# Optimization experiments

Hardware: AMD Instinct MI355X
Metric: run time of the kernel (lower is better)

Reference implementation:

```python
import jax, jax.numpy as jnp
import numpy as np

MARGIN = 0.1
SCALE_POS = 2.0
SCALE_NEG = 50.0
THRESH = 0.5
EPS = 1e-5


def setup_inputs() -> dict:
    key = jax.random.key(0)
    k1, k2 = jax.random.split(key)
    feats = jax.random.normal(k1, (4096, 2, 192), dtype=jnp.float32)
    labels = jax.random.randint(k2, (4096,), 0, 4096, dtype=jnp.int64)
    return {"feats": feats, "labels": labels}


def reference(feats, labels):
    B, n_utt, D = feats.shape
    lab = jnp.repeat(labels, n_utt)            # [N]
    f = feats.reshape(-1, D)                   # [N, D]
    N = f.shape[0]

    sim = f @ f.T                              # [N, N]
    # F.normalize(sim): L2-normalize each row, eps=1e-12
    row_norm = jnp.maximum(jnp.linalg.norm(sim, axis=1, keepdims=True), 1e-12)
    S = sim / row_norm

    same = lab[None, :] == lab[:, None]        # [N, N]
    pos_mask = same & (S < 1.0 - EPS)          # pos_pair_ (includes self if < 1-eps)
    neg_mask = ~same                           # neg_pair_

    min_pos = jnp.min(jnp.where(pos_mask, S, jnp.inf), axis=1)    # per-row min(pos_pair_)
    max_neg = jnp.max(jnp.where(neg_mask, S, -jnp.inf), axis=1)   # per-row max(neg_pair_)

    neg_keep = neg_mask & (S > (min_pos - MARGIN)[:, None])
    pos_keep = pos_mask & (S < (max_neg + MARGIN)[:, None])

    has_neg = jnp.any(neg_keep, axis=1)
    has_pos = jnp.any(pos_keep, axis=1)
    valid = has_neg & has_pos

    pos_sum = jnp.sum(jnp.where(pos_keep, jnp.exp(-SCALE_POS * (S - THRESH)), 0.0), axis=1)
    neg_sum = jnp.sum(jnp.where(neg_keep, jnp.exp(SCALE_NEG * (S - THRESH)), 0.0), axis=1)

    row_loss = (1.0 / SCALE_POS) * jnp.log1p(pos_sum) + (1.0 / SCALE_NEG) * jnp.log1p(neg_sum)
    loss = jnp.sum(jnp.where(valid, row_loss, 0.0)) / N

    # prec1 = percent of rows skipped for having no surviving negatives
    prec1 = jnp.sum(~has_neg).astype(jnp.float32) * 100.0 / N
    return loss, prec1
```

## Files before the change

### kernel.cpp

```cpp
#include <hip/hip_runtime.h>
#include <math.h>

typedef float  f32x4  __attribute__((ext_vector_type(4)));
typedef int    int8v  __attribute__((ext_vector_type(8)));

constexpr float MARGIN    = 0.1f;
constexpr float SCALE_POS = 2.0f;
constexpr float SCALE_NEG = 50.0f;
constexpr float THRESH    = 0.5f;
constexpr float ONE_EPS   = 1.0f - 1e-5f;
constexpr float LOG2E     = 1.4426950408889634f;
constexpr float BC        = -(SCALE_NEG * THRESH * LOG2E);
constexpr float VCUT_COEF = (36.0674f - 30.0f) / (SCALE_NEG * LOG2E);

constexpr int D      = 192;
constexpr int KP     = 256;
constexpr int RT     = 4;
constexpr int RPW    = 64;
constexpr int RPB    = 256;
constexpr int CSPLIT = 16;

constexpr int NSLOT  = 32;
constexpr int CBLK   = 256;
constexpr int NTILES = CBLK / 16;
constexpr int NPAIR  = (NSLOT * (NSLOT - 1)) / 2;

constexpr int TILE_B8 = 4096;
constexpr int SCALE1  = 0x7f7f7f7f;

__device__ inline float fast_exp2(float x) {
#if __has_builtin(__builtin_amdgcn_exp2f)
  return __builtin_amdgcn_exp2f(x);
#else
  return exp2f(x);
#endif
}

__device__ inline void pin_frag8(int8v& v) {
  asm volatile("" : "+v"(v));
}

__global__ __launch_bounds__(1024) void k_prep(
    const float* __restrict__ f, unsigned char* __restrict__ pk8, int nrows,
    const int* __restrict__ labs, int* __restrict__ hist_g, int* __restrict__ offs_g,
    int* __restrict__ bucket, float* __restrict__ accum, int n)
{
  if (blockIdx.x < 64) {
    int gid = blockIdx.x * 1024 + threadIdx.x;
    int r = gid >> 3, j = gid & 7;
    if (r >= nrows) return;
    float x[32];
    if (j < 6) {
      const float* src = f + (size_t)r * D + j * 32;
#pragma unroll
      for (int i = 0; i < 8; ++i) {
        float4 v = *(const float4*)(src + i * 4);
        x[i * 4 + 0] = v.x; x[i * 4 + 1] = v.y; x[i * 4 + 2] = v.z; x[i * 4 + 3] = v.w;
      }
    } else {
#pragma unroll
      for (int i = 0; i < 32; ++i) x[i] = 0.f;
    }
    union { int s[8]; int8v v; } u;
#pragma unroll
    for (int i = 0; i < 8; ++i) {
      int p = __builtin_amdgcn_cvt_pk_fp8_f32(x[i * 4 + 0], x[i * 4 + 1], 0, false);
      p     = __builtin_amdgcn_cvt_pk_fp8_f32(x[i * 4 + 2], x[i * 4 + 3], p, true);
      u.s[i] = p;
    }
    int tile = r >> 4, c = r & 15, g = j >> 2, qq = j & 3;
    *(int8v*)(pk8 + (size_t)tile * TILE_B8 + g * 2048 + (qq * 16 + c) * 32) = u.v;
    return;
  }

  __shared__ int histL[4096];
  __shared__ int offsL[4096];
  __shared__ int scanb[1024];
  const int t = threadIdx.x;

  if (t < 3) accum[t] = 0.f;
  for (int i = t; i < 4096; i += 1024) histL[i] = 0;
  __syncthreads();
  for (int i = t; i < n; i += 1024) atomicAdd(&histL[labs[i]], 1);
  __syncthreads();
  int base = t * 4;
  int v[4]; int ls = 0;
  for (int k = 0; k < 4; ++k) { v[k] = ls; ls += histL[base + k]; }
  scanb[t] = ls;
  __syncthreads();
  for (int o = 1; o < 1024; o <<= 1) {
    int x = (t >= o) ? scanb[t - o] : 0;
    __syncthreads();
    scanb[t] += x;
    __syncthreads();
  }
  int ebase = scanb[t] - ls;
  for (int k = 0; k < 4; ++k) {
    offsL[base + k] = ebase + v[k];
    offs_g[base + k] = ebase + v[k];
    hist_g[base + k] = histL[base + k];
  }
  __syncthreads();
  for (int i = t; i < 4096; i += 1024) histL[i] = 0;
  __syncthreads();
  for (int i = t; i < n; i += 1024) {
    int lab = labs[i];
    int p = atomicAdd(&histL[lab], 1);
    bucket[offsL[lab] + p] = i;
  }
}

__global__ __launch_bounds__(256, 2) void k_pass1(
    const unsigned char* __restrict__ pk8, const int* __restrict__ labs,
    float* __restrict__ sumsqP, float* __restrict__ maxnegP, int N)
{
  __shared__ int   ldsLab[CBLK];
  __shared__ float colS[4][CBLK];
  __shared__ float colM[4][CBLK];

  const int tid  = threadIdx.x;
  const int lane = tid & 63;
  const int w    = tid >> 6;
  const int q    = lane >> 4;
  const int c    = lane & 15;

  int i, j;
  if ((int)blockIdx.x < NPAIR) {
    int t = blockIdx.x; i = 0;
    while (t >= NSLOT - 1 - i) { t -= NSLOT - 1 - i; ++i; }
    j = i + 1 + t;
  } else {
    i = j = blockIdx.x - NPAIR;
  }
  const bool offd = (i != j);
  const int rowbase = i * CBLK + w * RPW;
  const int ctile0  = j * NTILES;

  ldsLab[tid] = labs[(j * CBLK + tid) >> 1];

  int8v afr[RT][2];
#pragma unroll
  for (int rt = 0; rt < RT; ++rt)
#pragma unroll
    for (int g = 0; g < 2; ++g) {
      afr[rt][g] = *(const int8v*)(pk8 + (size_t)((rowbase >> 4) + rt) * TILE_B8 + g * 2048 + lane * 32);
      pin_frag8(afr[rt][g]);
    }

  int labrow[RT][4];
#pragma unroll
  for (int rt = 0; rt < RT; ++rt)
#pragma unroll
    for (int rr = 0; rr < 4; ++rr)
      labrow[rt][rr] = labs[(rowbase + rt * 16 + q * 4 + rr) >> 1];

  float ssq[RT][4], mxn[RT][4];
#pragma unroll
  for (int rt = 0; rt < RT; ++rt)
#pragma unroll
    for (int rr = 0; rr < 4; ++rr) { ssq[rt][rr] = 0.f; mxn[rt][rr] = -INFINITY; }

  __syncthreads();

  auto loadB = [&](int tile, int8v (&bf)[2]) {
    const unsigned char* bp = pk8 + (size_t)(ctile0 + tile) * TILE_B8 + lane * 32;
#pragma unroll
    for (int g = 0; g < 2; ++g) bf[g] = *(const int8v*)(bp + g * 2048);
  };
  auto compute = [&](const int8v (&bf)[2], int t) {
    const int labcol = ldsLab[t * 16 + c];
    f32x4 acc[RT];
#pragma unroll
    for (int rt = 0; rt < RT; ++rt) acc[rt] = 0.f;
#pragma unroll
    for (int g = 0; g < 2; ++g)
#pragma unroll
      for (int rt = 0; rt < RT; ++rt)
        acc[rt] = __builtin_amdgcn_mfma_scale_f32_16x16x128_f8f6f4(
            afr[rt][g], bf[g], acc[rt], 0, 0, 0, SCALE1, 0, SCALE1);
    float csA = 0.f, cmA = -INFINITY;
#pragma unroll
    for (int rt = 0; rt < RT; ++rt)
#pragma unroll
      for (int rr = 0; rr < 4; ++rr) {
        float v = acc[rt][rr];
        ssq[rt][rr] = fmaf(v, v, ssq[rt][rr]);
        float vm = (labrow[rt][rr] == labcol) ? -INFINITY : v;
        mxn[rt][rr] = fmaxf(mxn[rt][rr], vm);
        csA = fmaf(v, v, csA);
        cmA = fmaxf(cmA, vm);
      }
    if (offd) {
      csA += __shfl_xor(csA, 16, 64);
      csA += __shfl_xor(csA, 32, 64);
      cmA = fmaxf(cmA, __shfl_xor(cmA, 16, 64));
      cmA = fmaxf(cmA, __shfl_xor(cmA, 32, 64));
      if (q == 0) { colS[w][t * 16 + c] = csA; colM[w][t * 16 + c] = cmA; }
    }
  };

  int8v b0[2], b1[2];
  loadB(0, b0);
  for (int t = 0; t < NTILES; t += 2) {
    loadB(t + 1, b1);
    compute(b0, t);
    int nx = t + 2; nx = (nx < NTILES) ? nx : 0;
    loadB(nx, b0);
    compute(b1, t + 1);
  }

#pragma unroll
  for (int rt = 0; rt < RT; ++rt)
#pragma unroll
    for (int rr = 0; rr < 4; ++rr) {
      float s = ssq[rt][rr], m = mxn[rt][rr];
#pragma unroll
      for (int msk = 1; msk < 16; msk <<= 1) {
        s += __shfl_xor(s, msk, 64);
        m = fmaxf(m, __shfl_xor(m, msk, 64));
      }
      if (c == 0) {
        int row = rowbase + rt * 16 + q * 4 + rr;
        sumsqP[(size_t)j * N + row] = s;
        maxnegP[(size_t)j * N + row] = m;
      }
    }

  if (offd) {
    __syncthreads();
    float s4 = colS[0][tid] + colS[1][tid] + colS[2][tid] + colS[3][tid];
    float m4 = fmaxf(fmaxf(colM[0][tid], colM[1][tid]),
                     fmaxf(colM[2][tid], colM[3][tid]));
    const int colrow = j * CBLK + tid;
    sumsqP[(size_t)i * N + colrow] = s4;
    maxnegP[(size_t)i * N + colrow] = m4;
  }
}

__global__ void k_rowstats(
    const float* __restrict__ f, const int* __restrict__ labs,
    const float* __restrict__ sumsqP, const float* __restrict__ maxnegP,
    const int* __restrict__ offs, const int* __restrict__ hist, const int* __restrict__ bucket,
    float* __restrict__ nthr2, float* __restrict__ arow,
    float* __restrict__ validf, float* __restrict__ hasnegf, float* __restrict__ posloss,
    int N)
{
  const int lane = threadIdx.x & 63;
  const int row  = blockIdx.x * 4 + (threadIdx.x >> 6);

  float s = 0.f, m = -INFINITY;
  if (lane < NSLOT) {
    s = sumsqP[(size_t)lane * N + row];
    m = maxnegP[(size_t)lane * N + row];
  }
#pragma unroll
  for (int msk = 1; msk < 64; msk <<= 1) {
    s += __shfl_xor(s, msk, 64);
    m = fmaxf(m, __shfl_xor(m, msk, 64));
  }
  float nrm = fmaxf(sqrtf(s), 1e-12f);
  float inv = 1.0f / nrm;
  float maxnegS = m * inv;
  float posth = fminf(ONE_EPS, maxnegS + MARGIN);

  const int lab = labs[row >> 1];
  const int beg = offs[lab], cnt = hist[lab];
  const float* fi = f + (size_t)row * D;
  float x0 = fi[lane], x1 = fi[lane + 64], x2 = fi[lane + 128];

  float minp = INFINITY, psum = 0.f; int pcnt = 0;
  for (int t = 0; t < cnt; ++t) {
    int smp = bucket[beg + t];
#pragma unroll
    for (int u = 0; u < 2; ++u) {
      const float* fj = f + (size_t)(smp * 2 + u) * D;
      float p = x0 * fj[lane] + x1 * fj[lane + 64] + x2 * fj[lane + 128];
#pragma unroll
      for (int msk = 1; msk < 64; msk <<= 1) p += __shfl_xor(p, msk, 64);
      minp = fminf(minp, p);
      float S = p * inv;
      if (S < posth) {
        psum += fast_exp2((THRESH - S) * (SCALE_POS * LOG2E));
        pcnt++;
      }
    }
  }

  float minS = minp * inv;
  float min_pos = (minS < ONE_EPS) ? minS : INFINITY;
  bool hneg = maxnegS > (min_pos - MARGIN);
  bool valid = hneg && (pcnt > 0);
  if (lane == 0) {
    nthr2[row]   = fmaxf((min_pos - MARGIN) * nrm, VCUT_COEF * nrm);
    arow[row]    = inv * (SCALE_NEG * LOG2E);
    validf[row]  = valid ? 1.f : 0.f;
    hasnegf[row] = hneg ? 1.f : 0.f;
    posloss[row] = valid ? ((1.0f / SCALE_POS) * log1pf(psum)) : 0.f;
  }
}

__global__ __launch_bounds__(256, 2) void k_pass2(
    const unsigned char* __restrict__ pk8,
    const float* __restrict__ nthr2, const float* __restrict__ arow,
    const float* __restrict__ maxnegP,
    float* __restrict__ negsumP, int N, int cps)
{
  const int lane = threadIdx.x & 63;
  const int w    = threadIdx.x >> 6;
  const int q    = lane >> 4;
  const int c    = lane & 15;
  const int cs   = blockIdx.x & (CSPLIT - 1);
  const int rbb  = blockIdx.x / CSPLIT;
  const int rowbase = rbb * RPB + w * RPW;
  const int ctile0 = (cs * cps) >> 4;
  const int ntiles = cps >> 4;

  {
    int myrow = rowbase + lane;
    float mn = fmaxf(maxnegP[(size_t)(2 * cs) * N + myrow],
                     maxnegP[(size_t)(2 * cs + 1) * N + myrow]);
    float th = nthr2[myrow];
    unsigned long long bal = __ballot(mn > th);
    if (bal == 0ull) {
      negsumP[(size_t)cs * N + myrow] = 0.f;
      return;
    }
  }

  int8v afr[RT][2];
#pragma unroll
  for (int rt = 0; rt < RT; ++rt)
#pragma unroll
    for (int g = 0; g < 2; ++g) {
      afr[rt][g] = *(const int8v*)(pk8 + (size_t)((rowbase >> 4) + rt) * TILE_B8 + g * 2048 + lane * 32);
      pin_frag8(afr[rt][g]);
    }

  float nthrv[RT][4], arw[RT][4], ns[RT][4];
#pragma unroll
  for (int rt = 0; rt < RT; ++rt)
#pragma unroll
    for (int rr = 0; rr < 4; ++rr) {
      int row = rowbase + rt * 16 + q * 4 + rr;
      nthrv[rt][rr] = nthr2[row];
      arw[rt][rr]   = arow[row];
      ns[rt][rr]    = 0.f;
    }

  auto loadB = [&](int tile, int8v (&bf)[2]) {
    const unsigned char* bp = pk8 + (size_t)(ctile0 + tile) * TILE_B8 + lane * 32;
#pragma unroll
    for (int g = 0; g < 2; ++g) bf[g] = *(const int8v*)(bp + g * 2048);
  };
  auto compute = [&](const int8v (&bf)[2]) {
    f32x4 acc[RT];
#pragma unroll
    for (int rt = 0; rt < RT; ++rt) acc[rt] = 0.f;
#pragma unroll
    for (int g = 0; g < 2; ++g)
#pragma unroll
      for (int rt = 0; rt < RT; ++rt)
        acc[rt] = __builtin_amdgcn_mfma_scale_f32_16x16x128_f8f6f4(
            afr[rt][g], bf[g], acc[rt], 0, 0, 0, SCALE1, 0, SCALE1);
#pragma unroll
    for (int rt = 0; rt < RT; ++rt)
#pragma unroll
      for (int rr = 0; rr < 4; ++rr) {
        float v = acc[rt][rr];
        float e = fast_exp2(fmaf(v, arw[rt][rr], BC));
        ns[rt][rr] += (v > nthrv[rt][rr]) ? e : 0.f;
      }
  };

  int8v b0[2], b1[2];
  loadB(0, b0);
  for (int t = 0; t < ntiles; t += 2) {
    loadB(t + 1, b1);
    compute(b0);
    int nx = t + 2; nx = (nx < ntiles) ? nx : 0;
    loadB(nx, b0);
    compute(b1);
  }

#pragma unroll
  for (int rt = 0; rt < RT; ++rt)
#pragma unroll
    for (int rr = 0; rr < 4; ++rr) {
      float sv = ns[rt][rr];
#pragma unroll
      for (int msk = 1; msk < 16; msk <<= 1) sv += __shfl_xor(sv, msk, 64);
      if (c == 0) {
        int row = rowbase + rt * 16 + q * 4 + rr;
        negsumP[(size_t)cs * N + row] = sv;
      }
    }
}

__global__ void k_final(const float* __restrict__ negsumP, const float* __restrict__ posloss,
                        const float* __restrict__ validf, const float* __restrict__ hasnegf,
                        float* __restrict__ accum, float* __restrict__ out, int N)
{
  int i = blockIdx.x * blockDim.x + threadIdx.x;
  float lacc = 0.f, nacc = 0.f;
  if (i < N) {
    float nsum = 0.f;
    for (int cs2 = 0; cs2 < CSPLIT; ++cs2) nsum += negsumP[(size_t)cs2 * N + i];
    lacc = validf[i] * (posloss[i] + (1.0f / SCALE_NEG) * log1pf(nsum));
    nacc = 1.0f - hasnegf[i];
  }
#pragma unroll
  for (int msk = 1; msk < 64; msk <<= 1) {
    lacc += __shfl_xor(lacc, msk, 64);
    nacc += __shfl_xor(nacc, msk, 64);
  }
  __shared__ float sl[4], sn[4];
  __shared__ bool isLast;
  int wid = threadIdx.x >> 6, lane = threadIdx.x & 63;
  if (lane == 0) { sl[wid] = lacc; sn[wid] = nacc; }
  __syncthreads();
  if (threadIdx.x == 0) {
    float L = sl[0] + sl[1] + sl[2] + sl[3];
    float Nn = sn[0] + sn[1] + sn[2] + sn[3];
    atomicAdd(&accum[0], L);
    atomicAdd(&accum[1], Nn);
    __threadfence();
    int tkt = atomicAdd((int*)&accum[2], 1);
    isLast = (tkt == (int)gridDim.x - 1);
  }
  __syncthreads();
  if (isLast && threadIdx.x == 0) {
    __threadfence();
    out[0] = accum[0] / (float)N;
    out[1] = accum[1] * 100.0f / (float)N;
  }
}

extern "C" void kernel_launch(void* const* d_in, const int* in_sizes, int n_in,
                              void* d_out, int out_size, void* d_ws, size_t ws_size,
                              hipStream_t stream)
{
  (void)n_in; (void)out_size; (void)ws_size;
  const float* f    = (const float*)d_in[0];
  const int*   labs = (const int*)d_in[1];
  const int Bs = in_sizes[1];
  const int N  = 2 * Bs;

  char* ws = (char*)d_ws;
  size_t off = 0;
  auto alloc = [&](size_t bytes) -> void* {
    void* p = ws + off;
    off += (bytes + 255) & ~(size_t)255;
    return p;
  };
  unsigned char* pk8 = (unsigned char*)alloc((size_t)N * KP);
  float* sumsqP  = (float*)alloc((size_t)NSLOT * N * sizeof(float));
  float* maxnegP = (float*)alloc((size_t)NSLOT * N * sizeof(float));
  float* negsumP = sumsqP;
  float* nthr2   = (float*)alloc((size_t)N * sizeof(float));
  float* arow    = (float*)alloc((size_t)N * sizeof(float));
  float* validf  = (float*)alloc((size_t)N * sizeof(float));
  float* hasnegf = (float*)alloc((size_t)N * sizeof(float));
  float* posloss = (float*)alloc((size_t)N * sizeof(float));
  int* hist   = (int*)alloc((size_t)Bs * sizeof(int));
  int* offs   = (int*)alloc((size_t)Bs * sizeof(int));
  int* bucket = (int*)alloc((size_t)Bs * sizeof(int));
  float* accum = (float*)alloc(4 * sizeof(float));

  k_prep<<<65, 1024, 0, stream>>>(f, pk8, N, labs, hist, offs, bucket, accum, Bs);

  k_pass1<<<NPAIR + NSLOT, 256, 0, stream>>>(pk8, labs, sumsqP, maxnegP, N);
  k_rowstats<<<N / 4, 256, 0, stream>>>(f, labs, sumsqP, maxnegP, offs, hist, bucket,
                                        nthr2, arow, validf, hasnegf, posloss, N);
  const int cps   = N / CSPLIT;
  const int grid2 = (N / RPB) * CSPLIT;
  k_pass2<<<grid2, 256, 0, stream>>>(pk8, nthr2, arow, maxnegP, negsumP, N, cps);
  k_final<<<N / 256, 256, 0, stream>>>(negsumP, posloss, validf, hasnegf, accum, (float*)d_out, N);
}
```

Baseline: 106.0 us.

## Split pass1 tile pairs into column halves and double pass2 column split

Each symmetric block-pair in pass1 is now split across two workgroups, each handling half of the 256 column tiles. Row and column partial sums go to separate buffers, indexed so rowstats and pass2 can pick the right source. Pass2's column split doubles to 32 so each block handles one 256-column slab, which lines up the early-skip check with pass1's per-slab maxneg partials. This is meant to raise parallelism and occupancy on the many-CU GPU. In exchange, partial-buffer traffic and the number of reduction slots grow.

Result: slower. 112.1 us (+5.7%).

```diff
diff --git a/kernel.cpp b/kernel.cpp
--- a/kernel.cpp
+++ b/kernel.cpp
@@ -18,11 +18,12 @@
 constexpr int RT     = 4;
 constexpr int RPW    = 64;
 constexpr int RPB    = 256;
-constexpr int CSPLIT = 16;
+constexpr int CSPLIT = 32;
 
 constexpr int NSLOT  = 32;
 constexpr int CBLK   = 256;
 constexpr int NTILES = CBLK / 16;
+constexpr int HT     = 8;
 constexpr int NPAIR  = (NSLOT * (NSLOT - 1)) / 2;
 
 constexpr int TILE_B8 = 4096;
@@ -112,11 +113,12 @@
 
 __global__ __launch_bounds__(256, 2) void k_pass1(
     const unsigned char* __restrict__ pk8, const int* __restrict__ labs,
-    float* __restrict__ sumsqP, float* __restrict__ maxnegP, int N)
-{
-  __shared__ int   ldsLab[CBLK];
-  __shared__ float colS[4][CBLK];
-  __shared__ float colM[4][CBLK];
+    float* __restrict__ rowPs, float* __restrict__ rowPm,
+    float* __restrict__ colPs, float* __restrict__ colPm, int N)
+{
+  __shared__ int   ldsLab[128];
+  __shared__ float colS[4][128];
+  __shared__ float colM[4][128];
 
   const int tid  = threadIdx.x;
   const int lane = tid & 63;
@@ -124,19 +126,21 @@
   const int q    = lane >> 4;
   const int c    = lane & 15;
 
+  const int pid = blockIdx.x >> 1;
+  const int h   = blockIdx.x & 1;
   int i, j;
-  if ((int)blockIdx.x < NPAIR) {
-    int t = blockIdx.x; i = 0;
+  if (pid < NPAIR) {
+    int t = pid; i = 0;
     while (t >= NSLOT - 1 - i) { t -= NSLOT - 1 - i; ++i; }
     j = i + 1 + t;
   } else {
-    i = j = blockIdx.x - NPAIR;
+    i = j = pid - NPAIR;
   }
   const bool offd = (i != j);
   const int rowbase = i * CBLK + w * RPW;
-  const int ctile0  = j * NTILES;
-
-  ldsLab[tid] = labs[(j * CBLK + tid) >> 1];
+  const int ctile0  = j * NTILES + h * HT;
+
+  if (tid < 128) ldsLab[tid] = labs[(j * CBLK + h * 128 + tid) >> 1];
 
   int8v afr[RT][2];
 #pragma unroll
@@ -201,14 +205,15 @@
 
   int8v b0[2], b1[2];
   loadB(0, b0);
-  for (int t = 0; t < NTILES; t += 2) {
+  for (int t = 0; t < HT; t += 2) {
     loadB(t + 1, b1);
     compute(b0, t);
-    int nx = t + 2; nx = (nx < NTILES) ? nx : 0;
+    int nx = t + 2; nx = (nx < HT) ? nx : 0;
     loadB(nx, b0);
     compute(b1, t + 1);
   }
 
+  const int fslot = 2 * j + h;
 #pragma unroll
   for (int rt = 0; rt < RT; ++rt)
 #pragma unroll
@@ -221,25 +226,28 @@
       }
       if (c == 0) {
         int row = rowbase + rt * 16 + q * 4 + rr;
-        sumsqP[(size_t)j * N + row] = s;
-        maxnegP[(size_t)j * N + row] = m;
+        rowPs[(size_t)fslot * N + row] = s;
+        rowPm[(size_t)fslot * N + row] = m;
       }
     }
 
   if (offd) {
     __syncthreads();
-    float s4 = colS[0][tid] + colS[1][tid] + colS[2][tid] + colS[3][tid];
-    float m4 = fmaxf(fmaxf(colM[0][tid], colM[1][tid]),
-                     fmaxf(colM[2][tid], colM[3][tid]));
-    const int colrow = j * CBLK + tid;
-    sumsqP[(size_t)i * N + colrow] = s4;
-    maxnegP[(size_t)i * N + colrow] = m4;
+    if (tid < 128) {
+      float s4 = colS[0][tid] + colS[1][tid] + colS[2][tid] + colS[3][tid];
+      float m4 = fmaxf(fmaxf(colM[0][tid], colM[1][tid]),
+                       fmaxf(colM[2][tid], colM[3][tid]));
+      const int colrow = j * CBLK + h * 128 + tid;
+      colPs[(size_t)i * N + colrow] = s4;
+      colPm[(size_t)i * N + colrow] = m4;
+    }
   }
 }
 
 __global__ void k_rowstats(
     const float* __restrict__ f, const int* __restrict__ labs,
-    const float* __restrict__ sumsqP, const float* __restrict__ maxnegP,
+    const float* __restrict__ rowPs, const float* __restrict__ rowPm,
+    const float* __restrict__ colPs, const float* __restrict__ colPm,
     const int* __restrict__ offs, const int* __restrict__ hist, const int* __restrict__ bucket,
     float* __restrict__ nthr2, float* __restrict__ arow,
     float* __restrict__ validf, float* __restrict__ hasnegf, float* __restrict__ posloss,
@@ -247,11 +255,16 @@
 {
   const int lane = threadIdx.x & 63;
   const int row  = blockIdx.x * 4 + (threadIdx.x >> 6);
+  const int b    = row >> 8;
 
   float s = 0.f, m = -INFINITY;
-  if (lane < NSLOT) {
-    s = sumsqP[(size_t)lane * N + row];
-    m = maxnegP[(size_t)lane * N + row];
+  if (lane >= 2 * b) {
+    s += rowPs[(size_t)lane * N + row];
+    m = fmaxf(m, rowPm[(size_t)lane * N + row]);
+  }
+  if (lane < b) {
+    s += colPs[(size_t)lane * N + row];
+    m = fmaxf(m, colPm[(size_t)lane * N + row]);
   }
 #pragma unroll
   for (int msk = 1; msk < 64; msk <<= 1) {
@@ -302,8 +315,8 @@
 __global__ __launch_bounds__(256, 2) void k_pass2(
     const unsigned char* __restrict__ pk8,
     const float* __restrict__ nthr2, const float* __restrict__ arow,
-    const float* __restrict__ maxnegP,
-    float* __restrict__ negsumP, int N, int cps)
+    const float* __restrict__ rowPm, const float* __restrict__ colPm,
+    float* __restrict__ negsumP, int N)
 {
   const int lane = threadIdx.x & 63;
   const int w    = threadIdx.x >> 6;
@@ -312,13 +325,16 @@
   const int cs   = blockIdx.x & (CSPLIT - 1);
   const int rbb  = blockIdx.x / CSPLIT;
   const int rowbase = rbb * RPB + w * RPW;
-  const int ctile0 = (cs * cps) >> 4;
-  const int ntiles = cps >> 4;
+  const int ctile0 = cs * NTILES;
+  const int ntiles = NTILES;
 
   {
     int myrow = rowbase + lane;
-    float mn = fmaxf(maxnegP[(size_t)(2 * cs) * N + myrow],
-                     maxnegP[(size_t)(2 * cs + 1) * N + myrow]);
+    int b = myrow >> 8;
+    float mn = (cs >= b)
+        ? fmaxf(rowPm[(size_t)(2 * cs) * N + myrow],
+                rowPm[(size_t)(2 * cs + 1) * N + myrow])
+        : colPm[(size_t)cs * N + myrow];
     float th = nthr2[myrow];
     unsigned long long bal = __ballot(mn > th);
     if (bal == 0ull) {
@@ -453,9 +469,11 @@
     return p;
   };
   unsigned char* pk8 = (unsigned char*)alloc((size_t)N * KP);
-  float* sumsqP  = (float*)alloc((size_t)NSLOT * N * sizeof(float));
-  float* maxnegP = (float*)alloc((size_t)NSLOT * N * sizeof(float));
-  float* negsumP = sumsqP;
+  float* rowPs  = (float*)alloc((size_t)64 * N * sizeof(float));
+  float* rowPm  = (float*)alloc((size_t)64 * N * sizeof(float));
+  float* colPs  = (float*)alloc((size_t)NSLOT * N * sizeof(float));
+  float* colPm  = (float*)alloc((size_t)NSLOT * N * sizeof(float));
+  float* negsumP = (float*)alloc((size_t)CSPLIT * N * sizeof(float));
   float* nthr2   = (float*)alloc((size_t)N * sizeof(float));
   float* arow    = (float*)alloc((size_t)N * sizeof(float));
   float* validf  = (float*)alloc((size_t)N * sizeof(float));
@@ -468,11 +486,11 @@
 
   k_prep<<<65, 1024, 0, stream>>>(f, pk8, N, labs, hist, offs, bucket, accum, Bs);
 
-  k_pass1<<<NPAIR + NSLOT, 256, 0, stream>>>(pk8, labs, sumsqP, maxnegP, N);
-  k_rowstats<<<N / 4, 256, 0, stream>>>(f, labs, sumsqP, maxnegP, offs, hist, bucket,
+  k_pass1<<<2 * NPAIR + 2 * NSLOT, 256, 0, stream>>>(pk8, labs, rowPs, rowPm, colPs, colPm, N);
+  k_rowstats<<<N / 4, 256, 0, stream>>>(f, labs, rowPs, rowPm, colPs, colPm,
+                                        offs, hist, bucket,
                                         nthr2, arow, validf, hasnegf, posloss, N);
-  const int cps   = N / CSPLIT;
   const int grid2 = (N / RPB) * CSPLIT;
-  k_pass2<<<grid2, 256, 0, stream>>>(pk8, nthr2, arow, maxnegP, negsumP, N, cps);
+  k_pass2<<<grid2, 256, 0, stream>>>(pk8, nthr2, arow, rowPm, colPm, negsumP, N);
   k_final<<<N / 256, 256, 0, stream>>>(negsumP, posloss, validf, hasnegf, accum, (float*)d_out, N);
 }
```

## Triple-buffer B tiles in pass1 and defer column reduction to LDS

Applied to the files above, without the earlier changes.

In the fused similarity pass, the double-buffered B-tile loop becomes a fully unrolled triple-buffered loop that prefetches two tiles ahead, so global loads can overlap more MFMA work. The per-tile cross-lane shuffle reduction for column statistics is replaced by storing each quad's partials to a larger LDS array and reducing them once at the end. The min-occupancy hint in launch_bounds is dropped so the compiler can use more registers. In exchange it uses more registers and LDS, which may reduce waves per CU.

Measured after the change: 151.5 us. +42.8%, slower.

```diff
diff --git a/kernel.cpp b/kernel.cpp
--- a/kernel.cpp
+++ b/kernel.cpp
@@ -110,13 +110,13 @@
   }
 }
 
-__global__ __launch_bounds__(256, 2) void k_pass1(
+__global__ __launch_bounds__(256) void k_pass1(
     const unsigned char* __restrict__ pk8, const int* __restrict__ labs,
     float* __restrict__ sumsqP, float* __restrict__ maxnegP, int N)
 {
   __shared__ int   ldsLab[CBLK];
-  __shared__ float colS[4][CBLK];
-  __shared__ float colM[4][CBLK];
+  __shared__ float colS[4][4][CBLK];
+  __shared__ float colM[4][4][CBLK];
 
   const int tid  = threadIdx.x;
   const int lane = tid & 63;
@@ -191,22 +191,19 @@
         cmA = fmaxf(cmA, vm);
       }
     if (offd) {
-      csA += __shfl_xor(csA, 16, 64);
-      csA += __shfl_xor(csA, 32, 64);
-      cmA = fmaxf(cmA, __shfl_xor(cmA, 16, 64));
-      cmA = fmaxf(cmA, __shfl_xor(cmA, 32, 64));
-      if (q == 0) { colS[w][t * 16 + c] = csA; colM[w][t * 16 + c] = cmA; }
+      colS[w][q][t * 16 + c] = csA;
+      colM[w][q][t * 16 + c] = cmA;
     }
   };
 
-  int8v b0[2], b1[2];
-  loadB(0, b0);
-  for (int t = 0; t < NTILES; t += 2) {
-    loadB(t + 1, b1);
-    compute(b0, t);
-    int nx = t + 2; nx = (nx < NTILES) ? nx : 0;
-    loadB(nx, b0);
-    compute(b1, t + 1);
+  int8v bb[3][2];
+  loadB(0, bb[0]);
+  loadB(1, bb[1]);
+#pragma unroll
+  for (int t = 0; t < NTILES; ++t) {
+    int nx = t + 2; nx = (nx < NTILES) ? nx : nx - NTILES;
+    loadB(nx, bb[(t + 2) % 3]);
+    compute(bb[t % 3], t);
   }
 
 #pragma unroll
@@ -228,9 +225,14 @@
 
   if (offd) {
     __syncthreads();
-    float s4 = colS[0][tid] + colS[1][tid] + colS[2][tid] + colS[3][tid];
-    float m4 = fmaxf(fmaxf(colM[0][tid], colM[1][tid]),
-                     fmaxf(colM[2][tid], colM[3][tid]));
+    float s4 = 0.f, m4 = -INFINITY;
+#pragma unroll
+    for (int ww = 0; ww < 4; ++ww)
+#pragma unroll
+      for (int qq = 0; qq < 4; ++qq) {
+        s4 += colS[ww][qq][tid];
+        m4 = fmaxf(m4, colM[ww][qq][tid]);
+      }
     const int colrow = j * CBLK + tid;
     sumsqP[(size_t)i * N + colrow] = s4;
     maxnegP[(size_t)i * N + colrow] = m4;
```
